# Performance work log

Hardware: AMD Instinct MI355X
Metric: run time of the kernel (lower is better)

Reference implementation:

```python
import jax, jax.numpy as jnp
import numpy as np

GAMMA = 0.5

def _rbf_gram(a, b):
    # exp(-gamma * ||a - b||^2), computed via the expanded quadratic form.
    # a: [N, d], b: [M, d] -> [N, M]
    a2 = jnp.sum(a * a, axis=-1)                      # [N]
    b2 = jnp.sum(b * b, axis=-1)                      # [M]
    sq = a2[:, None] + b2[None, :] - 2.0 * (a @ b.T)  # [N, M]
    return jnp.exp(-GAMMA * jnp.maximum(sq, 0.0))


def setup_inputs() -> dict:
    key = jax.random.key(0)
    kx, kp = jax.random.split(key)
    x = jax.random.normal(kx, (32768, 16), dtype=jnp.float32)
    particles = jax.random.normal(kp, (8192, 16), dtype=jnp.float32)
    return {"x": x, "particles": particles}


def reference(x, particles):
    n_p = particles.shape[0]
    # p=None, norm=True -> px = ones(N_x) / N_x
    px = jnp.ones(x.shape[0], dtype=x.dtype) / x.shape[0]
    t1 = jnp.mean(_rbf_gram(particles, particles))           # mean over [N_p, N_p]
    t2 = 2.0 * jnp.sum(px @ _rbf_gram(x, particles)) / n_p   # weighted row-sum of [N_x, N_p]
    return t1 - t2
```

## Files before the change

### kernel.cpp

```cpp
#include <hip/hip_runtime.h>
#include <hip/hip_bf16.h>

#define THREADS 256
#define DIM 16

typedef __attribute__((ext_vector_type(8))) short bf16x8;
typedef __attribute__((ext_vector_type(16))) float f32x16;
typedef __attribute__((ext_vector_type(2))) float f32x2;

__device__ __forceinline__ float rawexp2(float a) { return __builtin_amdgcn_exp2f(a); }

__global__ __launch_bounds__(THREADS) void prep_kernel(
    const float* __restrict__ x, int nx,
    const float* __restrict__ p, int np,
    short* __restrict__ xbs, float* __restrict__ xn,
    short* __restrict__ pbs, short* __restrict__ pb,
    float* __restrict__ pn, float* __restrict__ pfp)
{
    const float L2E  = 1.44269504088896340736f;
    const float HL2E = 0.72134752044448170368f;
    int i = blockIdx.x * THREADS + threadIdx.x;
    const float* src; short* ds; short* dp; float* dn; float* df;
    if (i < nx) {
        src = x + (size_t)i * DIM; ds = xbs + (size_t)i * DIM;
        dp = nullptr; dn = xn + i; df = nullptr;
    } else if (i < nx + np) {
        int j = i - nx;
        src = p + (size_t)j * DIM; ds = pbs + (size_t)j * DIM;
        dp = pb + (size_t)j * DIM; dn = pn + j; df = pfp + j;
    } else {
        return;
    }

    float nrm = 0.f;
    bf16x8 plo, phi, slo, shi;
#pragma unroll
    for (int k = 0; k < DIM; ++k) {
        unsigned u = __float_as_uint(src[k]);
        unsigned short r = (unsigned short)((u + 0x7FFFu + ((u >> 16) & 1u)) >> 16);
        float fr = __uint_as_float((unsigned)r << 16);
        nrm = fmaf(fr, fr, nrm);
        unsigned us = __float_as_uint(L2E * fr);
        unsigned short rs = (unsigned short)((us + 0x7FFFu + ((us >> 16) & 1u)) >> 16);
        if (k < 8) { plo[k] = (short)r; slo[k] = (short)rs; }
        else       { phi[k - 8] = (short)r; shi[k - 8] = (short)rs; }
    }
    *(bf16x8*)ds = slo; *((bf16x8*)ds + 1) = shi;
    if (dp) { *(bf16x8*)dp = plo; *((bf16x8*)dp + 1) = phi; }
    float ns = -HL2E * nrm;
    *dn = ns;
    if (df) *df = rawexp2(ns);
}

__device__ __forceinline__ void consume_tile(const f32x16& d, float f, f32x2& acc)
{
    f32x2 e0 = { rawexp2(d[0]),  rawexp2(d[1])  };
    f32x2 e1 = { rawexp2(d[2]),  rawexp2(d[3])  };
    f32x2 e2 = { rawexp2(d[4]),  rawexp2(d[5])  };
    f32x2 e3 = { rawexp2(d[6]),  rawexp2(d[7])  };
    f32x2 e4 = { rawexp2(d[8]),  rawexp2(d[9])  };
    f32x2 e5 = { rawexp2(d[10]), rawexp2(d[11]) };
    f32x2 e6 = { rawexp2(d[12]), rawexp2(d[13]) };
    f32x2 e7 = { rawexp2(d[14]), rawexp2(d[15]) };

    f32x2 s0 = e0 + e1;
    f32x2 s1 = e2 + e3;
    f32x2 s2 = e4 + e5;
    f32x2 s3 = e6 + e7;
    f32x2 u0 = s0 + s1;
    f32x2 u1 = s2 + s3;
    f32x2 t  = u0 + u1;
    f32x2 pf2 = {f, f};
    acc = t * pf2 + acc;
}

__device__ __forceinline__ float gram_phase(
    const short* __restrict__ rowsb, const float* __restrict__ rown,
    const short* __restrict__ colsb, const float* __restrict__ colpf,
    int row0, int ct0, int ntiles, int l31, int half)
{
    bf16x8 afrag = *(const bf16x8*)(rowsb + (size_t)(row0 + l31) * DIM + half * 8);

    f32x16 cseed;
#pragma unroll
    for (int r = 0; r < 16; ++r) {
        int rrow = (r & 3) + 8 * (r >> 2) + 4 * half;
        cseed[r] = rown[row0 + rrow];
    }

    const short* bptr = colsb + ((size_t)ct0 * 32 + l31) * DIM + half * 8;
    const float* fptr = colpf + ct0 * 32 + l31;
    const size_t bstride = (size_t)32 * DIM;

    bf16x8 b0 = *(const bf16x8*)bptr;
    bf16x8 b1 = *(const bf16x8*)(bptr + bstride);
    float  f0 = fptr[0];
    float  f1 = fptr[32];

    f32x16 d0 = __builtin_amdgcn_mfma_f32_32x32x16_bf16(afrag, b0, cseed, 0, 0, 0);
    f32x16 d1 = __builtin_amdgcn_mfma_f32_32x32x16_bf16(afrag, b1, cseed, 0, 0, 0);

    f32x2 acc = {0.f, 0.f};

#pragma unroll 1
    for (int t = 0; t + 2 < ntiles; t += 2) {
        bf16x8 bn0 = *(const bf16x8*)(bptr + (size_t)(t + 2) * bstride);
        float  fn0 = fptr[(t + 2) * 32];
        bf16x8 bn1 = *(const bf16x8*)(bptr + (size_t)(t + 3) * bstride);
        float  fn1 = fptr[(t + 3) * 32];

        consume_tile(d0, f0, acc);
        d0 = __builtin_amdgcn_mfma_f32_32x32x16_bf16(afrag, bn0, cseed, 0, 0, 0);
        consume_tile(d1, f1, acc);
        d1 = __builtin_amdgcn_mfma_f32_32x32x16_bf16(afrag, bn1, cseed, 0, 0, 0);

        f0 = fn0; f1 = fn1;
    }
    consume_tile(d0, f0, acc);
    consume_tile(d1, f1, acc);
    return acc.x + acc.y;
}

__global__ __launch_bounds__(THREADS) void gram_fused_kernel(
    const short* __restrict__ xbs, const float* __restrict__ xn,
    const short* __restrict__ pbs, const short* __restrict__ pb,
    const float* __restrict__ pn, const float* __restrict__ pfp,
    int nrt_p, int n1,
    int nrt_x, int n2,
    double sc1, double sc2,
    double* __restrict__ partials)
{
    const int lane = threadIdx.x & 63;
    const int wv   = threadIdx.x >> 6;
    const int l31  = lane & 31;
    const int half = lane >> 5;
    const int w    = blockIdx.x * (THREADS / 64) + wv;

    const int rt1 = w & (nrt_p - 1);
    const int c10 = (w / nrt_p) * n1;
    float acc1 = gram_phase(pbs, pn, pb, pfp, rt1 * 32, c10, n1, l31, half);

    const int rt2 = w & (nrt_x - 1);
    const int c20 = (w / nrt_x) * n2;
    float acc2 = gram_phase(xbs, xn, pb, pfp, rt2 * 32, c20, n2, l31, half);

    double v = (double)acc1 * sc1 - (double)acc2 * sc2;
#pragma unroll
    for (int off = 32; off > 0; off >>= 1) v += __shfl_down(v, off);

    __shared__ double sred[THREADS / 64];
    if (lane == 0) sred[wv] = v;
    __syncthreads();
    if (threadIdx.x == 0) {
        double tot = 0.0;
#pragma unroll
        for (int q = 0; q < THREADS / 64; ++q) tot += sred[q];
        partials[blockIdx.x] = tot;
    }
}

__global__ __launch_bounds__(THREADS) void finalize_kernel(
    const double* __restrict__ partials, int n, float* __restrict__ out)
{
    double v = 0.0;
    for (int i = threadIdx.x; i < n; i += THREADS) v += partials[i];
#pragma unroll
    for (int off = 32; off > 0; off >>= 1) v += __shfl_down(v, off);

    __shared__ double sred[THREADS / 64];
    const int lane = threadIdx.x & 63;
    const int wid = threadIdx.x >> 6;
    if (lane == 0) sred[wid] = v;
    __syncthreads();
    if (threadIdx.x == 0) {
        double tot = 0.0;
#pragma unroll
        for (int q = 0; q < THREADS / 64; ++q) tot += sred[q];
        out[0] = (float)tot;
    }
}

extern "C" void kernel_launch(void* const* d_in, const int* in_sizes, int n_in,
                              void* d_out, int out_size, void* d_ws, size_t ws_size,
                              hipStream_t stream) {
    const float* x = (const float*)d_in[0];
    const float* particles = (const float*)d_in[1];
    float* out = (float*)d_out;

    const int NX = in_sizes[0] / DIM;
    const int NP = in_sizes[1] / DIM;

    const int nrt_x = NX / 32;
    const int nrt_p = NP / 32;

    const int NBLOCKS = 1024;
    const int WAVES = NBLOCKS * (THREADS / 64);
    const int n1 = (nrt_p * nrt_p) / WAVES;
    const int n2 = (nrt_x * nrt_p) / WAVES;

    char* ws = (char*)d_ws;
    double* partials = (double*)ws;
    float*  xn  = (float*)(ws + 16384);
    float*  pn  = (float*)(ws + 147456);
    float*  pfp = (float*)(ws + 180224);
    short*  xbs = (short*)(ws + 212992);
    short*  pbs = (short*)(ws + 1261568);
    short*  pb  = (short*)(ws + 1523712);

    const int nprep = (NX + NP + THREADS - 1) / THREADS;
    prep_kernel<<<nprep, THREADS, 0, stream>>>(x, NX, particles, NP,
                                               xbs, xn, pbs, pb, pn, pfp);

    gram_fused_kernel<<<NBLOCKS, THREADS, 0, stream>>>(
        xbs, xn, pbs, pb, pn, pfp,
        nrt_p, n1, nrt_x, n2,
        1.0 / ((double)NP * (double)NP),
        2.0 / ((double)NX * (double)NP),
        partials);

    finalize_kernel<<<1, THREADS, 0, stream>>>(partials, NBLOCKS, out);
}
```

Before: 49.65 us.

## Exploit symmetry of particle Gram matrix by computing only upper-triangular tiles

Computes only the upper-triangular 32x32 tiles of the symmetric particle-particle Gram matrix and doubles the off-diagonal sum, roughly halving the work for term t1. Triangle rows are paired (j with 255-j) so every wave gets an equal share of tiles. The tile loop is now single-tile pipelined with branches inside it, and the sizes are hardcoded (256 particle row tiles, 1024 x row tiles, 64 column tiles), so the kernel only works for the current input shapes.

Result: faster. 47.34 us (median of 2 runs) (-4.6%).

```diff
diff --git a/kernel.cpp b/kernel.cpp
--- a/kernel.cpp
+++ b/kernel.cpp
@@ -121,12 +121,54 @@
     return acc.x + acc.y;
 }
 
+__device__ __forceinline__ void tri_run(
+    const short* __restrict__ rowsb, const float* __restrict__ rown,
+    const short* __restrict__ colsb, const float* __restrict__ colpf,
+    int rt, int ct0, int len, bool diagFirst, int l31, int half,
+    f32x2& accD, f32x2& accU)
+{
+    if (len <= 0) return;
+    const int row0 = rt * 32;
+    bf16x8 afrag = *(const bf16x8*)(rowsb + (size_t)(row0 + l31) * DIM + half * 8);
+
+    f32x16 cseed;
+#pragma unroll
+    for (int r = 0; r < 16; ++r) {
+        int rrow = (r & 3) + 8 * (r >> 2) + 4 * half;
+        cseed[r] = rown[row0 + rrow];
+    }
+
+    const short* bptr = colsb + ((size_t)ct0 * 32 + l31) * DIM + half * 8;
+    const float* fptr = colpf + ct0 * 32 + l31;
+    const size_t bstride = (size_t)32 * DIM;
+
+    bf16x8 bC = *(const bf16x8*)bptr;
+    float  fC = fptr[0];
+    f32x16 d = __builtin_amdgcn_mfma_f32_32x32x16_bf16(afrag, bC, cseed, 0, 0, 0);
+
+#pragma unroll 1
+    for (int t = 0; t < len; ++t) {
+        bf16x8 bN; float fN;
+        if (t + 1 < len) {
+            bN = *(const bf16x8*)(bptr + (size_t)(t + 1) * bstride);
+            fN = fptr[(t + 1) * 32];
+        }
+        if (diagFirst && t == 0) {
+            consume_tile(d, fC, accD);
+        } else {
+            consume_tile(d, fC, accU);
+        }
+        if (t + 1 < len) {
+            d = __builtin_amdgcn_mfma_f32_32x32x16_bf16(afrag, bN, cseed, 0, 0, 0);
+            fC = fN;
+        }
+    }
+}
+
 __global__ __launch_bounds__(THREADS) void gram_fused_kernel(
     const short* __restrict__ xbs, const float* __restrict__ xn,
     const short* __restrict__ pbs, const short* __restrict__ pb,
     const float* __restrict__ pn, const float* __restrict__ pfp,
-    int nrt_p, int n1,
-    int nrt_x, int n2,
     double sc1, double sc2,
     double* __restrict__ partials)
 {
@@ -136,15 +178,42 @@
     const int half = lane >> 5;
     const int w    = blockIdx.x * (THREADS / 64) + wv;
 
-    const int rt1 = w & (nrt_p - 1);
-    const int c10 = (w / nrt_p) * n1;
-    float acc1 = gram_phase(pbs, pn, pb, pfp, rt1 * 32, c10, n1, l31, half);
-
-    const int rt2 = w & (nrt_x - 1);
-    const int c20 = (w / nrt_x) * n2;
-    float acc2 = gram_phase(xbs, xn, pb, pfp, rt2 * 32, c20, n2, l31, half);
-
-    double v = (double)acc1 * sc1 - (double)acc2 * sc2;
+    f32x2 accD = {0.f, 0.f}, accU = {0.f, 0.f};
+    {
+        const int j = w >> 5;
+        const int k = w & 31;
+        const int s   = (k == 0) ? 0 : 8 * k + 1;
+        const int cnt = (k == 0) ? 9 : 8;
+        const int m = 256 - j;
+
+        {
+            const int lo = s;
+            const int hi = (s + cnt < m) ? (s + cnt) : m;
+            const int lenA = hi - lo;
+            if (lenA > 0)
+                tri_run(pbs, pn, pb, pfp, j, j + lo, lenA, lo == 0,
+                        l31, half, accD, accU);
+        }
+        {
+            const int lo = (s > m) ? s : m;
+            const int hi = s + cnt;
+            const int lenB = hi - lo;
+            if (lenB > 0) {
+                const int i2 = lo - m;
+                tri_run(pbs, pn, pb, pfp, 255 - j, (255 - j) + i2, lenB,
+                        i2 == 0, l31, half, accD, accU);
+            }
+        }
+    }
+    float t1d = accD.x + accD.y;
+    float t1u = accU.x + accU.y;
+
+    const int rt2 = w & 1023;
+    const int c20 = (w >> 10) * 64;
+    float acc2 = gram_phase(xbs, xn, pb, pfp, rt2 * 32, c20, 64, l31, half);
+
+    double v = ((double)t1d + 2.0 * (double)t1u) * sc1
+             - (double)acc2 * sc2;
 #pragma unroll
     for (int off = 32; off > 0; off >>= 1) v += __shfl_down(v, off);
 
@@ -190,13 +259,7 @@
     const int NX = in_sizes[0] / DIM;
     const int NP = in_sizes[1] / DIM;
 
-    const int nrt_x = NX / 32;
-    const int nrt_p = NP / 32;
-
     const int NBLOCKS = 1024;
-    const int WAVES = NBLOCKS * (THREADS / 64);
-    const int n1 = (nrt_p * nrt_p) / WAVES;
-    const int n2 = (nrt_x * nrt_p) / WAVES;
 
     char* ws = (char*)d_ws;
     double* partials = (double*)ws;
@@ -213,7 +276,6 @@
 
     gram_fused_kernel<<<NBLOCKS, THREADS, 0, stream>>>(
         xbs, xn, pbs, pb, pn, pfp,
-        nrt_p, n1, nrt_x, n2,
         1.0 / ((double)NP * (double)NP),
         2.0 / ((double)NX * (double)NP),
         partials);
```
